# Kernel tuning notes

Hardware: AMD Instinct MI355X
Metric: run time of the kernel (lower is better)

## Reference

```python
import jax, jax.numpy as jnp
import numpy as np

B, S, T = 4096, 512, 3
E, C_ENT, C_INT = 32, 4, 10


def setup_inputs() -> dict:
    key = jax.random.key(0)
    ks = jax.random.split(key, 9)
    lengths = jax.random.randint(ks[0], (B,), S // 2, S + 1)
    attention_mask = jnp.arange(S)[None, :] < lengths[:, None]  # [B,S] bool, contiguous from t=0
    return {
        "emission_score": jax.random.normal(ks[1], (B, S, T), dtype=jnp.float32),
        "attention_mask": attention_mask,
        "seq_labels": jax.random.randint(ks[2], (B, S), 0, T),
        "entity_logit": jax.random.normal(ks[3], (B, E, C_ENT), dtype=jnp.float32),
        "entity_labels": jax.random.randint(ks[4], (B, E), 0, C_ENT),
        "intent_logit": jax.random.normal(ks[5], (B, C_INT), dtype=jnp.float32),
        "intent_labels": jax.random.randint(ks[6], (B,), 0, C_INT),
        "start_transitions": jax.random.normal(ks[7], (T,), dtype=jnp.float32) * 0.1,
        "end_transitions": jax.random.normal(ks[8], (T,), dtype=jnp.float32) * 0.1,
        "transitions": jax.random.normal(jax.random.fold_in(key, 99), (T, T), dtype=jnp.float32) * 0.1,
    }


def crf_nll(emissions, mask, tags, start_t, end_t, trans):
    # emissions [B,S,T], mask bool [B,S] (mask[:,0] all True), tags int [B,S]
    maskf = mask.astype(emissions.dtype)
    # ---- numerator: score of gold path ----
    em_scores = jnp.take_along_axis(emissions, tags[..., None], axis=2)[..., 0]  # [B,S]
    trans_scores = trans[tags[:, :-1], tags[:, 1:]]  # [B,S-1]
    score = start_t[tags[:, 0]] + em_scores[:, 0]
    score = score + jnp.sum((trans_scores + em_scores[:, 1:]) * maskf[:, 1:], axis=1)
    last_idx = jnp.sum(mask, axis=1).astype(jnp.int32) - 1  # [B]
    last_tags = jnp.take_along_axis(tags, last_idx[:, None], axis=1)[:, 0]
    score = score + end_t[last_tags]
    # ---- denominator: forward algorithm (log partition) ----
    alpha0 = start_t[None, :] + emissions[:, 0]  # [B,T]

    def step(alpha, inp):
        em_t, m_t = inp  # [B,T], [B] bool
        # logsumexp over previous tag: [B,T_prev,1] + [T_prev,T] + [B,1,T]
        nxt = jax.nn.logsumexp(alpha[:, :, None] + trans[None, :, :] + em_t[:, None, :], axis=1)
        alpha = jnp.where(m_t[:, None], nxt, alpha)
        return alpha, None

    alpha, _ = jax.lax.scan(step, alpha0,
                            (jnp.swapaxes(emissions[:, 1:], 0, 1), jnp.swapaxes(mask[:, 1:], 0, 1)))
    denom = jax.nn.logsumexp(alpha + end_t[None, :], axis=1)  # [B]
    return jnp.mean(denom - score)


def cross_entropy(logits, labels, ignore_index=None):
    logp = jax.nn.log_softmax(logits, axis=-1)
    nll = -jnp.take_along_axis(logp, labels[:, None], axis=1)[:, 0]
    if ignore_index is None:
        return jnp.mean(nll)
    valid = (labels != ignore_index).astype(logits.dtype)
    return jnp.sum(nll * valid) / jnp.maximum(jnp.sum(valid), 1.0)


def reference(emission_score, attention_mask, seq_labels, entity_logit, entity_labels,
              intent_logit, intent_labels, start_transitions, end_transitions, transitions):
    loss1 = crf_nll(emission_score, attention_mask, seq_labels,
                    start_transitions, end_transitions, transitions)
    loss2 = cross_entropy(entity_logit.reshape(-1, entity_logit.shape[-1]),
                          entity_labels.reshape(-1), ignore_index=0)
    loss3 = cross_entropy(intent_logit.reshape(-1, intent_logit.shape[-1]),
                          intent_labels.reshape(-1))
    loss = (loss1 + loss2 + loss3) / 3.0
    return jnp.stack([loss, loss1, loss2, loss3])
```

## Files before the change

### kernel.cpp

```cpp
#include <hip/hip_runtime.h>

#define BB 4096
#define SS 512
#define EE 32
#define C_ENT 4
#define C_INT 10

#define ROWS_PER_BLOCK 4
#define NBLK (BB / ROWS_PER_BLOCK)

#define P_CRF 64
#define P_EN  (P_CRF + NBLK)
#define P_EC  (P_EN + NBLK)
#define P_IN  (P_EC + NBLK)


__device__ __forceinline__ float wave_sum(float v) {
#pragma unroll
    for (int off = 32; off > 0; off >>= 1) v += __shfl_down(v, off, 64);
    return v;
}

__device__ __forceinline__ float trsel(const float tr[9], int tp, int t) {
    float r0 = (tp == 0) ? tr[0] : (tp == 1) ? tr[3] : tr[6];
    float r1 = (tp == 0) ? tr[1] : (tp == 1) ? tr[4] : tr[7];
    float r2 = (tp == 0) ? tr[2] : (tp == 1) ? tr[5] : tr[8];
    return (t == 0) ? r0 : (t == 1) ? r1 : r2;
}

__global__ __launch_bounds__(256) void fused_kernel(
    const float* __restrict__ em_all, const int* __restrict__ mask_all,
    const int* __restrict__ tags_all,
    const float* __restrict__ ent_logits, const int* __restrict__ ent_labels,
    const float* __restrict__ int_logits, const int* __restrict__ int_labels,
    const float* __restrict__ start_t, const float* __restrict__ end_t,
    const float* __restrict__ trans, float* __restrict__ ws) {
    const int tid = threadIdx.x;
    const int wave = tid >> 6, lane = tid & 63;
    const int b = blockIdx.x * ROWS_PER_BLOCK + wave;

    float tr[9], etr[9];
#pragma unroll
    for (int i = 0; i < 9; ++i) { tr[i] = trans[i]; etr[i] = __expf(tr[i]); }

    const int4* mk4 = (const int4*)(mask_all + (size_t)b * SS);
    int4 ma = mk4[lane], mb = mk4[64 + lane];
    int L = ma.x + ma.y + ma.z + ma.w + mb.x + mb.y + mb.z + mb.w;
#pragma unroll
    for (int off = 1; off < 64; off <<= 1) L += __shfl_xor(L, off, 64);

    const int4* tg4 = (const int4*)(tags_all + (size_t)b * SS);
    int4 ta = tg4[2 * lane], tb = tg4[2 * lane + 1];
    int tg[9] = {ta.x, ta.y, ta.z, ta.w, tb.x, tb.y, tb.z, tb.w, 0};
    tg[8] = __shfl_down(tg[0], 1, 64);

    const float4* em4 = (const float4*)(em_all + (size_t)b * (SS * 3));
    float er[28];
#pragma unroll
    for (int i = 0; i < 6; ++i) {
        float4 v = em4[6 * lane + i];
        er[4 * i] = v.x; er[4 * i + 1] = v.y; er[4 * i + 2] = v.z; er[4 * i + 3] = v.w;
    }
    {
        float4 v = (lane < 63) ? em4[6 * lane + 6] : make_float4(0.f, 0.f, 0.f, 0.f);
        er[24] = v.x; er[25] = v.y; er[26] = v.z; er[27] = v.w;
    }

    const int count = min(max(L - 1 - 8 * lane, 0), 8);
    float M[9];
    float lsc = 0.f;
    float score_part = 0.f;

    if (count > 0) {
        float e0 = er[3], e1 = er[4], e2 = er[5];
        float x0 = __expf(e0), x1 = __expf(e1), x2 = __expf(e2);
#pragma unroll
        for (int r = 0; r < 3; ++r) {
            M[r * 3 + 0] = etr[r * 3 + 0] * x0;
            M[r * 3 + 1] = etr[r * 3 + 1] * x1;
            M[r * 3 + 2] = etr[r * 3 + 2] * x2;
        }
        int t = tg[1], tp = tg[0];
        score_part = trsel(tr, tp, t) + ((t == 0) ? e0 : (t == 1) ? e1 : e2);
    }
#pragma unroll
    for (int i = 1; i < 8; ++i) {
        if (i < count) {
            float e0 = er[3 * i + 3], e1 = er[3 * i + 4], e2 = er[3 * i + 5];
            float x0 = __expf(e0), x1 = __expf(e1), x2 = __expf(e2);
            float P[9];
#pragma unroll
            for (int r = 0; r < 3; ++r) {
                float m0 = M[r * 3 + 0], m1 = M[r * 3 + 1], m2 = M[r * 3 + 2];
                P[r * 3 + 0] = (m0 * etr[0] + m1 * etr[3] + m2 * etr[6]) * x0;
                P[r * 3 + 1] = (m0 * etr[1] + m1 * etr[4] + m2 * etr[7]) * x1;
                P[r * 3 + 2] = (m0 * etr[2] + m1 * etr[5] + m2 * etr[8]) * x2;
            }
#pragma unroll
            for (int e = 0; e < 9; ++e) M[e] = P[e];
            int t = tg[i + 1], tp = tg[i];
            score_part += trsel(tr, tp, t) + ((t == 0) ? e0 : (t == 1) ? e1 : e2);
        }
    }
    if (count > 0) {
        float mx = M[0];
#pragma unroll
        for (int e = 1; e < 9; ++e) mx = fmaxf(mx, M[e]);
        float inv = 1.0f / mx;
#pragma unroll
        for (int e = 0; e < 9; ++e) M[e] *= inv;
        lsc = __logf(mx);
    } else {
#pragma unroll
        for (int e = 0; e < 9; ++e) M[e] = 0.f;
        M[0] = M[4] = M[8] = 1.f;
    }

#pragma unroll
    for (int off = 1; off < 64; off <<= 1) {
        float R[9];
#pragma unroll
        for (int e = 0; e < 9; ++e) R[e] = __shfl_down(M[e], off, 64);
        float rs = __shfl_down(lsc, off, 64);
        float P[9];
#pragma unroll
        for (int r = 0; r < 3; ++r) {
            float m0 = M[r * 3 + 0], m1 = M[r * 3 + 1], m2 = M[r * 3 + 2];
            P[r * 3 + 0] = m0 * R[0] + m1 * R[3] + m2 * R[6];
            P[r * 3 + 1] = m0 * R[1] + m1 * R[4] + m2 * R[7];
            P[r * 3 + 2] = m0 * R[2] + m1 * R[5] + m2 * R[8];
        }
        float mx = P[0];
#pragma unroll
        for (int e = 1; e < 9; ++e) mx = fmaxf(mx, P[e]);
        float inv = 1.0f / mx;
#pragma unroll
        for (int e = 0; e < 9; ++e) M[e] = P[e] * inv;
        lsc = lsc + rs + __logf(mx);
    }

    float sc = wave_sum(score_part);

    __shared__ float s_crf[ROWS_PER_BLOCK];
    if (lane == 0) {
        float a0 = start_t[0] + er[0];
        float a1 = start_t[1] + er[1];
        float a2 = start_t[2] + er[2];
        float m0 = fmaxf(a0, fmaxf(a1, a2));
        float x0 = __expf(a0 - m0), x1 = __expf(a1 - m0), x2 = __expf(a2 - m0);
        float f0 = x0 * M[0] + x1 * M[3] + x2 * M[6];
        float f1 = x0 * M[1] + x1 * M[4] + x2 * M[7];
        float f2 = x0 * M[2] + x1 * M[5] + x2 * M[8];
        float e0 = end_t[0], e1 = end_t[1], e2 = end_t[2];
        float me = fmaxf(e0, fmaxf(e1, e2));
        float denom = __logf(f0 * __expf(e0 - me) + f1 * __expf(e1 - me) +
                             f2 * __expf(e2 - me)) + me + m0 + lsc;

        int t0 = tg[0];
        float score = sc + start_t[t0] +
                      ((t0 == 0) ? er[0] : (t0 == 1) ? er[1] : er[2]);
        int last_tag = tags_all[(size_t)b * SS + (L - 1)];
        score += end_t[last_tag];
        s_crf[wave] = denom - score;
    }

    const int gid = blockIdx.x * 256 + tid;
    float en = 0.f, ec = 0.f, inl = 0.f;
    if (gid < BB * EE) {
        float4 v = ((const float4*)ent_logits)[gid];
        int l = ent_labels[gid];
        float m = fmaxf(fmaxf(v.x, v.y), fmaxf(v.z, v.w));
        float lse = m + __logf(__expf(v.x - m) + __expf(v.y - m) +
                               __expf(v.z - m) + __expf(v.w - m));
        float selv = (l == 0) ? v.x : (l == 1) ? v.y : (l == 2) ? v.z : v.w;
        float valid = (l != 0) ? 1.f : 0.f;
        en = (lse - selv) * valid;
        ec = valid;
    }
    if (gid < BB) {
        const float2* p2 = (const float2*)(int_logits + (size_t)gid * C_INT);
        float x[C_INT];
#pragma unroll
        for (int i = 0; i < 5; ++i) {
            float2 v = p2[i];
            x[2 * i] = v.x; x[2 * i + 1] = v.y;
        }
        float m = x[0];
#pragma unroll
        for (int i = 1; i < C_INT; ++i) m = fmaxf(m, x[i]);
        float s = 0.f;
#pragma unroll
        for (int i = 0; i < C_INT; ++i) s += __expf(x[i] - m);
        float lse = m + __logf(s);
        int l = int_labels[gid];
        float selv = x[0];
#pragma unroll
        for (int i = 1; i < C_INT; ++i) selv = (l == i) ? x[i] : selv;
        inl = lse - selv;
    }

    en = wave_sum(en);
    ec = wave_sum(ec);
    inl = wave_sum(inl);

    __shared__ float s_en[4], s_ec[4], s_in[4];
    if (lane == 0) { s_en[wave] = en; s_ec[wave] = ec; s_in[wave] = inl; }
    __syncthreads();
    if (tid == 0) {
        float a = 0.f, p = 0.f, c = 0.f, d = 0.f;
#pragma unroll
        for (int w = 0; w < ROWS_PER_BLOCK; ++w) {
            a += s_crf[w]; p += s_en[w]; c += s_ec[w]; d += s_in[w];
        }
        ws[P_CRF + blockIdx.x] = a;
        ws[P_EN + blockIdx.x] = p;
        ws[P_EC + blockIdx.x] = c;
        ws[P_IN + blockIdx.x] = d;
    }
}

__global__ __launch_bounds__(256) void finalize_kernel(
    const float* __restrict__ ws, float* __restrict__ out) {
    const int tid = threadIdx.x;
    const int wave = tid >> 6, lane = tid & 63;
    float a = 0.f, p = 0.f, c = 0.f, d = 0.f;
    for (int i = tid; i < NBLK; i += 256) {
        a += ws[P_CRF + i];
        p += ws[P_EN + i];
        c += ws[P_EC + i];
        d += ws[P_IN + i];
    }
    a = wave_sum(a); p = wave_sum(p); c = wave_sum(c); d = wave_sum(d);
    __shared__ float s[4][4];
    if (lane == 0) { s[0][wave] = a; s[1][wave] = p; s[2][wave] = c; s[3][wave] = d; }
    __syncthreads();
    if (tid == 0) {
        float t0 = 0.f, t1 = 0.f, t2 = 0.f, t3 = 0.f;
#pragma unroll
        for (int w = 0; w < 4; ++w) {
            t0 += s[0][w]; t1 += s[1][w]; t2 += s[2][w]; t3 += s[3][w];
        }
        float l1 = t0 / (float)BB;
        float l2 = t1 / fmaxf(t2, 1.f);
        float l3 = t3 / (float)BB;
        out[0] = (l1 + l2 + l3) / 3.f;
        out[1] = l1;
        out[2] = l2;
        out[3] = l3;
    }
}

extern "C" void kernel_launch(void* const* d_in, const int* in_sizes, int n_in,
                              void* d_out, int out_size, void* d_ws, size_t ws_size,
                              hipStream_t stream) {
    const float* emission     = (const float*)d_in[0];
    const int*   mask         = (const int*)d_in[1];
    const int*   seq_labels   = (const int*)d_in[2];
    const float* entity_logit = (const float*)d_in[3];
    const int*   entity_lbl   = (const int*)d_in[4];
    const float* intent_logit = (const float*)d_in[5];
    const int*   intent_lbl   = (const int*)d_in[6];
    const float* start_t      = (const float*)d_in[7];
    const float* end_t        = (const float*)d_in[8];
    const float* trans        = (const float*)d_in[9];
    float* out = (float*)d_out;
    float* ws  = (float*)d_ws;

    fused_kernel<<<NBLK, 256, 0, stream>>>(emission, mask, seq_labels,
                                           entity_logit, entity_lbl,
                                           intent_logit, intent_lbl,
                                           start_t, end_t, trans, ws);
    finalize_kernel<<<1, 256, 0, stream>>>(ws, out);
}
```

Measured before the change: 113.6 us.

## Use per-step mask predicates and a ballot-based length to cut dependent reductions

Each lane now reads the mask entries aligned with its own 8 steps and predicates each transition step on its mask bit. This replaces the count computed from a full 6-stage shuffle reduction of the sequence length. The length L is now derived from a ballot of full 8-blocks plus one shuffle, which depends on the mask being a contiguous prefix. The trans load and exp are moved after the global loads, and the per-block partials are packed as a single float4 write and read back in finalize, cutting the long serial dependency chain before the scan.

```diff
diff --git a/kernel.cpp b/kernel.cpp
--- a/kernel.cpp
+++ b/kernel.cpp
@@ -9,10 +9,7 @@
 #define ROWS_PER_BLOCK 4
 #define NBLK (BB / ROWS_PER_BLOCK)
 
-#define P_CRF 64
-#define P_EN  (P_CRF + NBLK)
-#define P_EC  (P_EN + NBLK)
-#define P_IN  (P_EC + NBLK)
+#define P_BASE 64
 
 
 __device__ __forceinline__ float wave_sum(float v) {
@@ -39,21 +36,10 @@
     const int wave = tid >> 6, lane = tid & 63;
     const int b = blockIdx.x * ROWS_PER_BLOCK + wave;
 
-    float tr[9], etr[9];
-#pragma unroll
-    for (int i = 0; i < 9; ++i) { tr[i] = trans[i]; etr[i] = __expf(tr[i]); }
-
     const int4* mk4 = (const int4*)(mask_all + (size_t)b * SS);
-    int4 ma = mk4[lane], mb = mk4[64 + lane];
-    int L = ma.x + ma.y + ma.z + ma.w + mb.x + mb.y + mb.z + mb.w;
-#pragma unroll
-    for (int off = 1; off < 64; off <<= 1) L += __shfl_xor(L, off, 64);
-
+    int4 m0 = mk4[2 * lane], m1 = mk4[2 * lane + 1];
     const int4* tg4 = (const int4*)(tags_all + (size_t)b * SS);
     int4 ta = tg4[2 * lane], tb = tg4[2 * lane + 1];
-    int tg[9] = {ta.x, ta.y, ta.z, ta.w, tb.x, tb.y, tb.z, tb.w, 0};
-    tg[8] = __shfl_down(tg[0], 1, 64);
-
     const float4* em4 = (const float4*)(em_all + (size_t)b * (SS * 3));
     float er[28];
 #pragma unroll
@@ -66,35 +52,37 @@
         er[24] = v.x; er[25] = v.y; er[26] = v.z; er[27] = v.w;
     }
 
-    const int count = min(max(L - 1 - 8 * lane, 0), 8);
-    float M[9];
-    float lsc = 0.f;
+    float tr[9], etr[9];
+#pragma unroll
+    for (int i = 0; i < 9; ++i) { tr[i] = trans[i]; etr[i] = __expf(tr[i]); }
+
+    int v[8];
+    v[0] = m0.y; v[1] = m0.z; v[2] = m0.w;
+    v[3] = m1.x; v[4] = m1.y; v[5] = m1.z; v[6] = m1.w;
+    v[7] = (lane < 63) ? __shfl_down(m0.x, 1, 64) : 0;
+    int tg[9] = {ta.x, ta.y, ta.z, ta.w, tb.x, tb.y, tb.z, tb.w, 0};
+    tg[8] = __shfl_down(tg[0], 1, 64);
+
+    int s8 = m0.x + m0.y + m0.z + m0.w + m1.x + m1.y + m1.z + m1.w;
+    unsigned long long full = __ballot(s8 == 8);
+    int q = __popcll(full);
+    int r = __shfl(s8, q & 63, 64);
+    const int L = 8 * q + ((q < 64) ? r : 0);
+
+    float M[9] = {1.f, 0.f, 0.f, 0.f, 1.f, 0.f, 0.f, 0.f, 1.f};
     float score_part = 0.f;
-
-    if (count > 0) {
-        float e0 = er[3], e1 = er[4], e2 = er[5];
-        float x0 = __expf(e0), x1 = __expf(e1), x2 = __expf(e2);
-#pragma unroll
-        for (int r = 0; r < 3; ++r) {
-            M[r * 3 + 0] = etr[r * 3 + 0] * x0;
-            M[r * 3 + 1] = etr[r * 3 + 1] * x1;
-            M[r * 3 + 2] = etr[r * 3 + 2] * x2;
-        }
-        int t = tg[1], tp = tg[0];
-        score_part = trsel(tr, tp, t) + ((t == 0) ? e0 : (t == 1) ? e1 : e2);
-    }
-#pragma unroll
-    for (int i = 1; i < 8; ++i) {
-        if (i < count) {
+#pragma unroll
+    for (int i = 0; i < 8; ++i) {
+        if (v[i]) {
             float e0 = er[3 * i + 3], e1 = er[3 * i + 4], e2 = er[3 * i + 5];
             float x0 = __expf(e0), x1 = __expf(e1), x2 = __expf(e2);
             float P[9];
 #pragma unroll
-            for (int r = 0; r < 3; ++r) {
-                float m0 = M[r * 3 + 0], m1 = M[r * 3 + 1], m2 = M[r * 3 + 2];
-                P[r * 3 + 0] = (m0 * etr[0] + m1 * etr[3] + m2 * etr[6]) * x0;
-                P[r * 3 + 1] = (m0 * etr[1] + m1 * etr[4] + m2 * etr[7]) * x1;
-                P[r * 3 + 2] = (m0 * etr[2] + m1 * etr[5] + m2 * etr[8]) * x2;
+            for (int rr = 0; rr < 3; ++rr) {
+                float a0 = M[rr * 3 + 0], a1 = M[rr * 3 + 1], a2 = M[rr * 3 + 2];
+                P[rr * 3 + 0] = (a0 * etr[0] + a1 * etr[3] + a2 * etr[6]) * x0;
+                P[rr * 3 + 1] = (a0 * etr[1] + a1 * etr[4] + a2 * etr[7]) * x1;
+                P[rr * 3 + 2] = (a0 * etr[2] + a1 * etr[5] + a2 * etr[8]) * x2;
             }
 #pragma unroll
             for (int e = 0; e < 9; ++e) M[e] = P[e];
@@ -102,7 +90,8 @@
             score_part += trsel(tr, tp, t) + ((t == 0) ? e0 : (t == 1) ? e1 : e2);
         }
     }
-    if (count > 0) {
+    float lsc;
+    {
         float mx = M[0];
 #pragma unroll
         for (int e = 1; e < 9; ++e) mx = fmaxf(mx, M[e]);
@@ -110,10 +99,6 @@
 #pragma unroll
         for (int e = 0; e < 9; ++e) M[e] *= inv;
         lsc = __logf(mx);
-    } else {
-#pragma unroll
-        for (int e = 0; e < 9; ++e) M[e] = 0.f;
-        M[0] = M[4] = M[8] = 1.f;
     }
 
 #pragma unroll
@@ -124,11 +109,11 @@
         float rs = __shfl_down(lsc, off, 64);
         float P[9];
 #pragma unroll
-        for (int r = 0; r < 3; ++r) {
-            float m0 = M[r * 3 + 0], m1 = M[r * 3 + 1], m2 = M[r * 3 + 2];
-            P[r * 3 + 0] = m0 * R[0] + m1 * R[3] + m2 * R[6];
-            P[r * 3 + 1] = m0 * R[1] + m1 * R[4] + m2 * R[7];
-            P[r * 3 + 2] = m0 * R[2] + m1 * R[5] + m2 * R[8];
+        for (int rr = 0; rr < 3; ++rr) {
+            float a0 = M[rr * 3 + 0], a1 = M[rr * 3 + 1], a2 = M[rr * 3 + 2];
+            P[rr * 3 + 0] = a0 * R[0] + a1 * R[3] + a2 * R[6];
+            P[rr * 3 + 1] = a0 * R[1] + a1 * R[4] + a2 * R[7];
+            P[rr * 3 + 2] = a0 * R[2] + a1 * R[5] + a2 * R[8];
         }
         float mx = P[0];
 #pragma unroll
@@ -146,15 +131,15 @@
         float a0 = start_t[0] + er[0];
         float a1 = start_t[1] + er[1];
         float a2 = start_t[2] + er[2];
-        float m0 = fmaxf(a0, fmaxf(a1, a2));
-        float x0 = __expf(a0 - m0), x1 = __expf(a1 - m0), x2 = __expf(a2 - m0);
+        float mm = fmaxf(a0, fmaxf(a1, a2));
+        float x0 = __expf(a0 - mm), x1 = __expf(a1 - mm), x2 = __expf(a2 - mm);
         float f0 = x0 * M[0] + x1 * M[3] + x2 * M[6];
         float f1 = x0 * M[1] + x1 * M[4] + x2 * M[7];
         float f2 = x0 * M[2] + x1 * M[5] + x2 * M[8];
         float e0 = end_t[0], e1 = end_t[1], e2 = end_t[2];
         float me = fmaxf(e0, fmaxf(e1, e2));
         float denom = __logf(f0 * __expf(e0 - me) + f1 * __expf(e1 - me) +
-                             f2 * __expf(e2 - me)) + me + m0 + lsc;
+                             f2 * __expf(e2 - me)) + me + mm + lsc;
 
         int t0 = tg[0];
         float score = sc + start_t[t0] +
@@ -167,12 +152,12 @@
     const int gid = blockIdx.x * 256 + tid;
     float en = 0.f, ec = 0.f, inl = 0.f;
     if (gid < BB * EE) {
-        float4 v = ((const float4*)ent_logits)[gid];
+        float4 vv = ((const float4*)ent_logits)[gid];
         int l = ent_labels[gid];
-        float m = fmaxf(fmaxf(v.x, v.y), fmaxf(v.z, v.w));
-        float lse = m + __logf(__expf(v.x - m) + __expf(v.y - m) +
-                               __expf(v.z - m) + __expf(v.w - m));
-        float selv = (l == 0) ? v.x : (l == 1) ? v.y : (l == 2) ? v.z : v.w;
+        float m = fmaxf(fmaxf(vv.x, vv.y), fmaxf(vv.z, vv.w));
+        float lse = m + __logf(__expf(vv.x - m) + __expf(vv.y - m) +
+                               __expf(vv.z - m) + __expf(vv.w - m));
+        float selv = (l == 0) ? vv.x : (l == 1) ? vv.y : (l == 2) ? vv.z : vv.w;
         float valid = (l != 0) ? 1.f : 0.f;
         en = (lse - selv) * valid;
         ec = valid;
@@ -182,8 +167,8 @@
         float x[C_INT];
 #pragma unroll
         for (int i = 0; i < 5; ++i) {
-            float2 v = p2[i];
-            x[2 * i] = v.x; x[2 * i + 1] = v.y;
+            float2 vv = p2[i];
+            x[2 * i] = vv.x; x[2 * i + 1] = vv.y;
         }
         float m = x[0];
 #pragma unroll
@@ -212,10 +197,7 @@
         for (int w = 0; w < ROWS_PER_BLOCK; ++w) {
             a += s_crf[w]; p += s_en[w]; c += s_ec[w]; d += s_in[w];
         }
-        ws[P_CRF + blockIdx.x] = a;
-        ws[P_EN + blockIdx.x] = p;
-        ws[P_EC + blockIdx.x] = c;
-        ws[P_IN + blockIdx.x] = d;
+        ((float4*)(ws + P_BASE))[blockIdx.x] = make_float4(a, p, c, d);
     }
 }
 
@@ -223,16 +205,15 @@
     const float* __restrict__ ws, float* __restrict__ out) {
     const int tid = threadIdx.x;
     const int wave = tid >> 6, lane = tid & 63;
-    float a = 0.f, p = 0.f, c = 0.f, d = 0.f;
+    const float4* p = (const float4*)(ws + P_BASE);
+    float a = 0.f, pn = 0.f, c = 0.f, d = 0.f;
     for (int i = tid; i < NBLK; i += 256) {
-        a += ws[P_CRF + i];
-        p += ws[P_EN + i];
-        c += ws[P_EC + i];
-        d += ws[P_IN + i];
-    }
-    a = wave_sum(a); p = wave_sum(p); c = wave_sum(c); d = wave_sum(d);
+        float4 v = p[i];
+        a += v.x; pn += v.y; c += v.z; d += v.w;
+    }
+    a = wave_sum(a); pn = wave_sum(pn); c = wave_sum(c); d = wave_sum(d);
     __shared__ float s[4][4];
-    if (lane == 0) { s[0][wave] = a; s[1][wave] = p; s[2][wave] = c; s[3][wave] = d; }
+    if (lane == 0) { s[0][wave] = a; s[1][wave] = pn; s[2][wave] = c; s[3][wave] = d; }
     __syncthreads();
     if (tid == 0) {
         float t0 = 0.f, t1 = 0.f, t2 = 0.f, t3 = 0.f;
```

New measurement: 128.0 us. 12.7% more time.
